# Kernel optimization log

Measured on AMD Instinct MI355X. Metric: run time of the kernel, lower is better.

## Reference

```python
import jax, jax.numpy as jnp
import numpy as np

N = 50000
E = 800000
IN = 128
H = 128
OUT = 64
L = 2
THETA = 1.0
SCALE = 2.0


def setup_inputs() -> dict:
    key = jax.random.key(0)
    ks = jax.random.split(key, 12)
    g = lambda k, s: (jax.random.normal(k, s, jnp.float32) * 0.05)
    return {
        "x": jax.random.normal(ks[0], (N, IN), jnp.float32),
        "edge_index": jax.random.randint(ks[1], (2, E), 0, N),
        "mlp_w1": g(ks[2], (IN, 512)), "mlp_b1": jnp.zeros((512,), jnp.float32),
        "mlp_w2": g(ks[3], (512, 64)), "mlp_b2": jnp.zeros((64,), jnp.float32),
        "mlp_w3": g(ks[4], (64, OUT)), "mlp_b3": jnp.zeros((OUT,), jnp.float32),
        "parsing": jnp.ones((L, OUT, OUT), jnp.float32) / SCALE,
        "lin0_w": g(ks[5], (IN, H)), "lin0_b": jnp.zeros((H,), jnp.float32),
        "lin1_w": g(ks[6], (H, OUT)), "lin1_b": jnp.zeros((OUT,), jnp.float32),
        "conv_w1": g(ks[7], (L, H, H)),
        "conv_w2": g(ks[8], (L, H, H)),
    }


def reference(x, edge_index, mlp_w1, mlp_b1, mlp_w2, mlp_b2, mlp_w3, mlp_b3,
              parsing, lin0_w, lin0_b, lin1_w, lin1_b, conv_w1, conv_w2):
    row, col = edge_index[0], edge_index[1]  # start, end

    # --- learn_soft_edge3 (algebraically exact reduction of outer-product + bmm + diag) ---
    h = jax.nn.relu(x @ mlp_w1 + mlp_b1)
    h = jax.nn.relu(h @ mlp_w2 + mlp_b2)
    logits = h @ mlp_w3 + mlp_b3                      # [N, OUT]
    P = jax.nn.relu(SCALE * parsing[0])               # [OUT, OUT]
    # diag(outer(start,end) @ P)[e,c] = start[e,c] * (end @ P)[e,c]
    ew = jnp.sum(logits[row] * (logits @ P)[col], axis=1)  # [E]
    mean = ew.mean()
    var = jnp.var(ew, ddof=1)                          # torch.var is unbiased
    ew = (ew - mean) * jnp.sqrt(jnp.float32(1e-4) / var) + 1.0

    # --- GCN2 stack ---
    x0 = jax.nn.relu(x @ lin0_w + lin0_b)              # [N, H]
    # gcn_norm with self loops (weight 1)
    loop = jnp.arange(N)
    r = jnp.concatenate([row, loop])
    c = jnp.concatenate([col, loop])
    w = jnp.concatenate([ew, jnp.ones((N,), ew.dtype)])
    deg = jax.ops.segment_sum(w, c, num_segments=N)
    dinv = jnp.where(deg > 0, jax.lax.rsqrt(jnp.where(deg > 0, deg, 1.0)), 0.0)
    norm = dinv[r] * w * dinv[c]                       # [E+N]

    hcur = x0
    alpha = 0.0
    for ln in range(L):
        agg = jax.ops.segment_sum(norm[:, None] * hcur[r], c, num_segments=N)  # [N, H]
        agg = agg * (1.0 - alpha)
        x0a = alpha * x0
        beta = float(np.log(THETA / (ln + 1) + 1.0))
        out = (1.0 - beta) * agg + beta * (agg @ conv_w1[ln]) \
            + (1.0 - beta) * x0a + beta * (x0a @ conv_w2[ln])
        hcur = jax.nn.relu(out)
    return hcur @ lin1_w + lin1_b                      # [N, OUT]
```

## Files before the change

### kernel.cpp

```cpp
#include <hip/hip_runtime.h>
#include <hip/hip_bf16.h>
#include <hip/hip_fp16.h>
#include <math.h>

#define NN 50000
#define NE 800000

typedef __attribute__((ext_vector_type(8))) short bf16x8;
typedef __attribute__((ext_vector_type(4))) float f32x4;

__device__ __forceinline__ short f2bf(float f){
  unsigned u = __float_as_uint(f);
  unsigned r = (u + 0x7fffu + ((u >> 16) & 1u)) >> 16;
  return (short)r;
}
__device__ __forceinline__ float bf2f(short s){
  return __uint_as_float(((unsigned)(unsigned short)s) << 16);
}

__device__ __forceinline__ unsigned f2fp8(float f){
  __half h = __float2half(f * 0.00390625f);
  unsigned hb = (unsigned)__half_as_ushort(h);
  unsigned s = hb >> 15;
  unsigned mag = hb & 0x7fffu;
  mag = mag + 0x3fu + ((mag >> 7) & 1u);
  unsigned m8 = mag >> 7;
  if (m8 > 0x7eu) m8 = 0x7eu;
  return (s << 7) | m8;
}
__device__ __forceinline__ void fp8x4_dec(unsigned u, float2& lo, float2& hi){
  unsigned l = ((u & 0x80u) << 8) | ((u & 0x7fu) << 7)
             | ((u & 0x8000u) << 16) | ((u & 0x7f00u) << 15);
  unsigned h = ((u & 0x800000u) >> 8) | ((u & 0x7f0000u) >> 9)
             | (u & 0x80000000u) | ((u & 0x7f000000u) >> 1);
  __half2 hl = *(__half2*)&l;
  __half2 hh = *(__half2*)&h;
  lo = __half22float2(hl);
  hi = __half22float2(hh);
}
__device__ __forceinline__ float fp8_dot4(unsigned a, unsigned b){
  float2 al, ah, bl, bh;
  fp8x4_dec(a, al, ah); fp8x4_dec(b, bl, bh);
  return al.x*bl.x + al.y*bl.y + ah.x*bh.x + ah.y*bh.y;
}

__global__ __launch_bounds__(256) void zero_cnt_k(int* __restrict__ cnt, float* __restrict__ scal, int n){
  int i = blockIdx.x*256 + threadIdx.x;
  if (i < n) cnt[i] = 0;
  if (blockIdx.x == 0 && threadIdx.x < 16) scal[threadIdx.x] = 0.0f;
}

__global__ __launch_bounds__(256) void prep_k(const float* __restrict__ w1,
    const float* __restrict__ w2, const float* __restrict__ w3, const float* __restrict__ pars,
    const float* __restrict__ lin0w, const float* __restrict__ cw1, const float* __restrict__ lin1w,
    short* __restrict__ w1t, short* __restrict__ w2t, short* __restrict__ w3t, short* __restrict__ Pt,
    short* __restrict__ lin0wt, short* __restrict__ cw1t0, short* __restrict__ cw1t1,
    short* __restrict__ lin1wt){
  int idx = blockIdx.x*256 + threadIdx.x;
  if (idx < 65536){
    int n = idx >> 7, k = idx & 127;
    w1t[idx] = f2bf(w1[k*512 + n]);
  } else if (idx < 98304){
    int i = idx - 65536; int n = i >> 9, k = i & 511;
    w2t[i] = f2bf(w2[k*64 + n]);
  } else if (idx < 102400){
    int i = idx - 98304; int n = i >> 6, k = i & 63;
    w3t[i] = f2bf(w3[k*64 + n]);
  } else if (idx < 106496){
    int i = idx - 102400; int n = i >> 6, k = i & 63;
    Pt[i] = f2bf(fmaxf(2.f*pars[k*64 + n], 0.f));
  } else if (idx < 122880){
    int i = idx - 106496; int n = i >> 7, k = i & 127;
    lin0wt[i] = f2bf(lin0w[k*128 + n]);
  } else if (idx < 139264){
    int i = idx - 122880; int n = i >> 7, k = i & 127;
    cw1t0[i] = f2bf(cw1[k*128 + n]);
  } else if (idx < 155648){
    int i = idx - 139264; int n = i >> 7, k = i & 127;
    cw1t1[i] = f2bf(cw1[16384 + k*128 + n]);
  } else if (idx < 163840){
    int i = idx - 155648; int n = i >> 7, k = i & 127;
    lin1wt[i] = f2bf(lin1w[k*64 + n]);
  }
}

__global__ __launch_bounds__(256) void mlp_mfma_k(
    const float* __restrict__ x,
    const short* __restrict__ w1t, const float* __restrict__ b1,
    const short* __restrict__ w2t, const float* __restrict__ b2,
    const short* __restrict__ w3t, const float* __restrict__ b3,
    const short* __restrict__ Pt,
    unsigned char* __restrict__ lg8, unsigned char* __restrict__ lgp8,
    short* __restrict__ xb, int M)
{
  __shared__ short xs [32][136];
  __shared__ short h1s[32][520];
  __shared__ short h2s[32][72];
  __shared__ short lgs[32][72];
  const int t = threadIdx.x;
  const int wave = t >> 6, lane = t & 63;
  const int quad = lane >> 4, l16 = lane & 15;
  const int m0 = blockIdx.x * 32;

  for (int task = t; task < 512; task += 256){
    int row = task >> 4, c0 = (task & 15) * 8;
    float4 v0 = make_float4(0,0,0,0), v1 = v0;
    if (m0 + row < M){
      v0 = *(const float4*)(x + (size_t)(m0+row)*128 + c0);
      v1 = *(const float4*)(x + (size_t)(m0+row)*128 + c0 + 4);
    }
    bf16x8 s;
    s[0]=f2bf(v0.x); s[1]=f2bf(v0.y); s[2]=f2bf(v0.z); s[3]=f2bf(v0.w);
    s[4]=f2bf(v1.x); s[5]=f2bf(v1.y); s[6]=f2bf(v1.z); s[7]=f2bf(v1.w);
    *(bf16x8*)&xs[row][c0] = s;
  }
  __syncthreads();

  {
    f32x4 acc[2][8];
    #pragma unroll
    for (int mt=0;mt<2;mt++)
      #pragma unroll
      for (int nt=0;nt<8;nt++) acc[mt][nt] = (f32x4){0.f,0.f,0.f,0.f};
    for (int k0 = 0; k0 < 128; k0 += 32){
      bf16x8 a0 = *(const bf16x8*)&xs[l16     ][k0 + quad*8];
      bf16x8 a1 = *(const bf16x8*)&xs[16 + l16][k0 + quad*8];
      #pragma unroll
      for (int nt = 0; nt < 8; nt++){
        int n = wave*128 + nt*16 + l16;
        bf16x8 b = *(const bf16x8*)(w1t + (size_t)n*128 + k0 + quad*8);
        acc[0][nt] = __builtin_amdgcn_mfma_f32_16x16x32_bf16(a0, b, acc[0][nt], 0,0,0);
        acc[1][nt] = __builtin_amdgcn_mfma_f32_16x16x32_bf16(a1, b, acc[1][nt], 0,0,0);
      }
    }
    #pragma unroll
    for (int nt = 0; nt < 8; nt++){
      int n = wave*128 + nt*16 + l16;
      float bb = b1[n];
      #pragma unroll
      for (int mt = 0; mt < 2; mt++){
        #pragma unroll
        for (int r = 0; r < 4; r++){
          int row = mt*16 + quad*4 + r;
          h1s[row][n] = f2bf(fmaxf(acc[mt][nt][r] + bb, 0.f));
        }
      }
    }
  }
  __syncthreads();

  {
    f32x4 acc[2];
    acc[0] = (f32x4){0.f,0.f,0.f,0.f}; acc[1] = acc[0];
    const int n = wave*16 + l16;
    for (int k0 = 0; k0 < 512; k0 += 32){
      bf16x8 b  = *(const bf16x8*)(w2t + (size_t)n*512 + k0 + quad*8);
      bf16x8 a0 = *(const bf16x8*)&h1s[l16     ][k0 + quad*8];
      bf16x8 a1 = *(const bf16x8*)&h1s[16 + l16][k0 + quad*8];
      acc[0] = __builtin_amdgcn_mfma_f32_16x16x32_bf16(a0, b, acc[0], 0,0,0);
      acc[1] = __builtin_amdgcn_mfma_f32_16x16x32_bf16(a1, b, acc[1], 0,0,0);
    }
    float bb = b2[n];
    #pragma unroll
    for (int mt = 0; mt < 2; mt++)
      #pragma unroll
      for (int r = 0; r < 4; r++)
        h2s[mt*16 + quad*4 + r][n] = f2bf(fmaxf(acc[mt][r] + bb, 0.f));
  }
  __syncthreads();

  {
    f32x4 acc[2];
    acc[0] = (f32x4){0.f,0.f,0.f,0.f}; acc[1] = acc[0];
    const int n = wave*16 + l16;
    for (int k0 = 0; k0 < 64; k0 += 32){
      bf16x8 b  = *(const bf16x8*)(w3t + (size_t)n*64 + k0 + quad*8);
      bf16x8 a0 = *(const bf16x8*)&h2s[l16     ][k0 + quad*8];
      bf16x8 a1 = *(const bf16x8*)&h2s[16 + l16][k0 + quad*8];
      acc[0] = __builtin_amdgcn_mfma_f32_16x16x32_bf16(a0, b, acc[0], 0,0,0);
      acc[1] = __builtin_amdgcn_mfma_f32_16x16x32_bf16(a1, b, acc[1], 0,0,0);
    }
    float bb = b3[n];
    #pragma unroll
    for (int mt = 0; mt < 2; mt++)
      #pragma unroll
      for (int r = 0; r < 4; r++)
        lgs[mt*16 + quad*4 + r][n] = f2bf(acc[mt][r] + bb);
  }
  __syncthreads();

  {
    f32x4 acc[2];
    acc[0] = (f32x4){0.f,0.f,0.f,0.f}; acc[1] = acc[0];
    const int n = wave*16 + l16;
    for (int k0 = 0; k0 < 64; k0 += 32){
      bf16x8 b  = *(const bf16x8*)(Pt + (size_t)n*64 + k0 + quad*8);
      bf16x8 a0 = *(const bf16x8*)&lgs[l16     ][k0 + quad*8];
      bf16x8 a1 = *(const bf16x8*)&lgs[16 + l16][k0 + quad*8];
      acc[0] = __builtin_amdgcn_mfma_f32_16x16x32_bf16(a0, b, acc[0], 0,0,0);
      acc[1] = __builtin_amdgcn_mfma_f32_16x16x32_bf16(a1, b, acc[1], 0,0,0);
    }
    #pragma unroll
    for (int mt = 0; mt < 2; mt++)
      #pragma unroll
      for (int r = 0; r < 4; r++)
        h2s[mt*16 + quad*4 + r][n] = f2bf(acc[mt][r]);
  }
  __syncthreads();

  {
    int row = t >> 3, c0 = (t & 7) * 8;
    int gm = m0 + row;
    if (gm < M){
      const short* pl = &lgs[row][c0];
      const short* pp = &h2s[row][c0];
      unsigned a0 = 0, a1 = 0, b0 = 0, b1 = 0;
      #pragma unroll
      for (int j = 0; j < 4; j++){
        a0 |= f2fp8(bf2f(pl[j]))     << (8*j);
        a1 |= f2fp8(bf2f(pl[4+j]))   << (8*j);
        b0 |= f2fp8(bf2f(pp[j]))     << (8*j);
        b1 |= f2fp8(bf2f(pp[4+j]))   << (8*j);
      }
      uint2 av; av.x = a0; av.y = a1;
      uint2 bv; bv.x = b0; bv.y = b1;
      *(uint2*)(lg8  + (size_t)gm*64 + c0) = av;
      *(uint2*)(lgp8 + (size_t)gm*64 + c0) = bv;
    }
  }
  for (int task = t; task < 512; task += 256){
    int row = task >> 4, c0 = (task & 15) * 8;
    int gm = m0 + row;
    if (gm < M)
      *(bf16x8*)(xb + (size_t)gm*128 + c0) = *(const bf16x8*)&xs[row][c0];
  }
}

template<int NT, bool RELU, bool RESID, bool BF16OUT>
__global__ __launch_bounds__(256) void bgemm_k(
    const short* __restrict__ A, const short* __restrict__ Bt,
    const float* __restrict__ bias, const short* __restrict__ extra,
    float* __restrict__ C, short* __restrict__ Cb, int M, float beta)
{
  const int N = NT*64;
  __shared__ short As[32][136];
  const int t = threadIdx.x;
  const int wave = t >> 6, lane = t & 63;
  const int quad = lane >> 4, l16 = lane & 15;
  const int m0 = blockIdx.x * 32;

  for (int task = t; task < 512; task += 256){
    int row = task >> 4, c0 = (task & 15) * 8;
    bf16x8 v = {0,0,0,0,0,0,0,0};
    if (m0 + row < M) v = *(const bf16x8*)(A + (size_t)(m0+row)*128 + c0);
    *(bf16x8*)&As[row][c0] = v;
  }
  __syncthreads();

  f32x4 acc[2][NT];
  #pragma unroll
  for (int mt=0;mt<2;mt++)
    #pragma unroll
    for (int nt=0;nt<NT;nt++) acc[mt][nt] = (f32x4){0.f,0.f,0.f,0.f};

  #pragma unroll
  for (int k0 = 0; k0 < 128; k0 += 32){
    bf16x8 a0 = *(const bf16x8*)&As[l16     ][k0 + quad*8];
    bf16x8 a1 = *(const bf16x8*)&As[16 + l16][k0 + quad*8];
    #pragma unroll
    for (int nt = 0; nt < NT; nt++){
      int n = (wave*NT + nt)*16 + l16;
      bf16x8 b = *(const bf16x8*)(Bt + (size_t)n*128 + k0 + quad*8);
      acc[0][nt] = __builtin_amdgcn_mfma_f32_16x16x32_bf16(a0, b, acc[0][nt], 0,0,0);
      acc[1][nt] = __builtin_amdgcn_mfma_f32_16x16x32_bf16(a1, b, acc[1][nt], 0,0,0);
    }
  }

  #pragma unroll
  for (int nt = 0; nt < NT; nt++){
    int n = (wave*NT + nt)*16 + l16;
    float bb = (bias != nullptr) ? bias[n] : 0.f;
    #pragma unroll
    for (int mt = 0; mt < 2; mt++){
      #pragma unroll
      for (int r = 0; r < 4; r++){
        int gm = m0 + mt*16 + quad*4 + r;
        if (gm >= M) continue;
        float v = acc[mt][nt][r];
        if (RESID){
          float ex = bf2f(extra[(size_t)gm*N + n]);
          v = beta*v + (1.f - beta)*ex;
        }
        v += bb;
        if (RELU) v = fmaxf(v, 0.f);
        if (BF16OUT) Cb[(size_t)gm*N + n] = f2bf(v);
        else         C [(size_t)gm*N + n] = v;
      }
    }
  }
}

__global__ __launch_bounds__(256) void count_k(const int* __restrict__ col, int* __restrict__ cnt, int E){
  int e = blockIdx.x*256 + threadIdx.x;
  if (e < E) atomicAdd(&cnt[col[e]], 1);
}

__global__ __launch_bounds__(256) void scan_sums_k(const int* __restrict__ cnt, int* __restrict__ bsum, int n){
  __shared__ int s[256];
  const int t = threadIdx.x;
  int i = blockIdx.x*1024 + t*4;
  int4 v = make_int4(0,0,0,0);
  if (i + 3 < n) v = *(const int4*)(cnt + i);
  else {
    if (i   < n) v.x = cnt[i];
    if (i+1 < n) v.y = cnt[i+1];
    if (i+2 < n) v.z = cnt[i+2];
    if (i+3 < n) v.w = cnt[i+3];
  }
  s[t] = v.x + v.y + v.z + v.w;
  __syncthreads();
  for (int st = 128; st; st >>= 1){
    if (t < st) s[t] += s[t + st];
    __syncthreads();
  }
  if (t == 0) bsum[blockIdx.x] = s[0];
}

__global__ __launch_bounds__(64) void scan_bsum_k(int* __restrict__ bsum, int nb){
  int t = threadIdx.x;
  int own = (t < nb) ? bsum[t] : 0;
  int v = own;
  #pragma unroll
  for (int off = 1; off < 64; off <<= 1){
    int o = __shfl_up(v, off, 64);
    if (t >= off) v += o;
  }
  if (t < nb) bsum[t] = v - own;
}

__global__ __launch_bounds__(256) void scan_final_k(const int* __restrict__ cnt, const int* __restrict__ bsum,
    int* __restrict__ off, int* __restrict__ cursor, int n, int total){
  __shared__ int s[256];
  const int t = threadIdx.x;
  int i = blockIdx.x*1024 + t*4;
  int4 v = make_int4(0,0,0,0);
  if (i + 3 < n) v = *(const int4*)(cnt + i);
  else {
    if (i   < n) v.x = cnt[i];
    if (i+1 < n) v.y = cnt[i+1];
    if (i+2 < n) v.z = cnt[i+2];
    if (i+3 < n) v.w = cnt[i+3];
  }
  int tsum = v.x + v.y + v.z + v.w;
  s[t] = tsum;
  __syncthreads();
  #pragma unroll
  for (int st = 1; st < 256; st <<= 1){
    int a = (t >= st) ? s[t - st] : 0;
    __syncthreads();
    s[t] += a;
    __syncthreads();
  }
  int base = s[t] - tsum + bsum[blockIdx.x];
  int o0 = base, o1 = o0 + v.x, o2 = o1 + v.y, o3 = o2 + v.z;
  if (i   < n){ off[i]   = o0; cursor[i]   = o0; }
  if (i+1 < n){ off[i+1] = o1; cursor[i+1] = o1; }
  if (i+2 < n){ off[i+2] = o2; cursor[i+2] = o2; }
  if (i+3 < n){ off[i+3] = o3; cursor[i+3] = o3; }
  if (blockIdx.x == 0 && t == 0) off[n] = total;
}

__global__ __launch_bounds__(256) void scatter_k(const int* __restrict__ row, const int* __restrict__ col,
    int* __restrict__ cursor, int* __restrict__ csr_src, int* __restrict__ csr_dst, int E){
  int e = blockIdx.x*256 + threadIdx.x;
  if (e < E){
    int r = row[e], c = col[e];
    int slot = atomicAdd(&cursor[c], 1);
    csr_src[slot] = r;
    csr_dst[slot] = c;
  }
}

__global__ __launch_bounds__(256) void ew2_k(const unsigned char* __restrict__ lg8,
    const unsigned char* __restrict__ lgp8,
    const int* __restrict__ src, const int* __restrict__ dst,
    float* __restrict__ w, float* __restrict__ scal, int E){
  const int t = threadIdx.x;
  const int lane = t & 63, wid = t >> 6;
  const int g = lane >> 4, q = lane & 15;
  const int gid = (blockIdx.x*4 + wid)*4 + g;
  const int ngroups = gridDim.x*16;
  float s = 0.f, ss = 0.f;
  for (int base = gid*4; base < E; base += ngroups*4){
    int4 r4 = *(const int4*)(src + base);
    int4 c4 = *(const int4*)(dst + base);
    unsigned a0 = *(const unsigned*)(lg8  + (size_t)r4.x*64 + q*4);
    unsigned a1 = *(const unsigned*)(lg8  + (size_t)r4.y*64 + q*4);
    unsigned a2 = *(const unsigned*)(lg8  + (size_t)r4.z*64 + q*4);
    unsigned a3 = *(const unsigned*)(lg8  + (size_t)r4.w*64 + q*4);
    unsigned b0 = *(const unsigned*)(lgp8 + (size_t)c4.x*64 + q*4);
    unsigned b1 = *(const unsigned*)(lgp8 + (size_t)c4.y*64 + q*4);
    unsigned b2 = *(const unsigned*)(lgp8 + (size_t)c4.z*64 + q*4);
    unsigned b3 = *(const unsigned*)(lgp8 + (size_t)c4.w*64 + q*4);
    float v0 = fp8_dot4(a0, b0);
    float v1 = fp8_dot4(a1, b1);
    float v2 = fp8_dot4(a2, b2);
    float v3 = fp8_dot4(a3, b3);
    #pragma unroll
    for (int o = 1; o < 16; o <<= 1){
      v0 += __shfl_xor(v0, o); v1 += __shfl_xor(v1, o);
      v2 += __shfl_xor(v2, o); v3 += __shfl_xor(v3, o);
    }
    if (q == 0){
      float4 vv = make_float4(v0*65536.f, v1*65536.f, v2*65536.f, v3*65536.f);
      *(float4*)(w + base) = vv;
      s  += vv.x + vv.y + vv.z + vv.w;
      ss += vv.x*vv.x + vv.y*vv.y + vv.z*vv.z + vv.w*vv.w;
    }
  }
  #pragma unroll
  for (int o = 1; o < 64; o <<= 1){ s += __shfl_xor(s, o); ss += __shfl_xor(ss, o); }
  __shared__ float ls[4], lss[4];
  if (lane == 0){ ls[wid] = s; lss[wid] = ss; }
  __syncthreads();
  if (t == 0){
    atomicAdd(&scal[0], ls[0]+ls[1]+ls[2]+ls[3]);
    atomicAdd(&scal[1], lss[0]+lss[1]+lss[2]+lss[3]);
  }
}

__global__ void finalize_k(float* scal, int E){
  double sum = (double)scal[0], sumsq = (double)scal[1];
  double mean = sum / (double)E;
  double var  = (sumsq - sum*sum/(double)E) / (double)(E-1);
  scal[2] = (float)mean;
  scal[3] = (float)sqrt(1e-4 / var);
}

__global__ __launch_bounds__(256) void degnorm_k(float* __restrict__ w, const int* __restrict__ off,
    const float* __restrict__ scal, float* __restrict__ dinv, int Nn){
  int n = blockIdx.x*256 + threadIdx.x;
  if (n < Nn){
    float mean = scal[2], k = scal[3];
    int s = off[n], e = off[n+1];
    float d = 1.0f;
    for (int j = s; j < e; j++){
      float v = (w[j] - mean) * k + 1.0f;
      w[j] = v;
      d += v;
    }
    dinv[n] = (d > 0.f) ? rsqrtf(d) : 0.f;
  }
}

__global__ __launch_bounds__(256) void wfin_k(float* __restrict__ w, const int* __restrict__ src,
    const int* __restrict__ dst, const float* __restrict__ dinv, int E){
  int e = blockIdx.x*256 + threadIdx.x;
  if (e < E) w[e] = w[e] * dinv[dst[e]] * dinv[src[e]];
}

__global__ __launch_bounds__(256) void agg_gather_k(const short* __restrict__ hb,
    const int* __restrict__ off, const int* __restrict__ src, const float* __restrict__ w,
    const float* __restrict__ dinv, short* __restrict__ aggb, int Nn){
  int n = blockIdx.x*4 + (threadIdx.x >> 6);
  int lane = threadIdx.x & 63;
  if (n >= Nn) return;
  float d = dinv[n];
  short2 hv = *(const short2*)(hb + (size_t)n*128 + lane*2);
  float acc0 = d*d*bf2f(hv.x), acc1 = d*d*bf2f(hv.y);
  int s = off[n], e = off[n+1];
  int j = s;
  for (; j + 7 < e; j += 8){
    int4 i0 = *(const int4*)(src + j);
    int4 i1 = *(const int4*)(src + j + 4);
    float4 w0 = *(const float4*)(w + j);
    float4 w1 = *(const float4*)(w + j + 4);
    short2 h0 = *(const short2*)(hb + (size_t)i0.x*128 + lane*2);
    short2 h1 = *(const short2*)(hb + (size_t)i0.y*128 + lane*2);
    short2 h2 = *(const short2*)(hb + (size_t)i0.z*128 + lane*2);
    short2 h3 = *(const short2*)(hb + (size_t)i0.w*128 + lane*2);
    short2 h4 = *(const short2*)(hb + (size_t)i1.x*128 + lane*2);
    short2 h5 = *(const short2*)(hb + (size_t)i1.y*128 + lane*2);
    short2 h6 = *(const short2*)(hb + (size_t)i1.z*128 + lane*2);
    short2 h7 = *(const short2*)(hb + (size_t)i1.w*128 + lane*2);
    acc0 += w0.x*bf2f(h0.x) + w0.y*bf2f(h1.x) + w0.z*bf2f(h2.x) + w0.w*bf2f(h3.x)
          + w1.x*bf2f(h4.x) + w1.y*bf2f(h5.x) + w1.z*bf2f(h6.x) + w1.w*bf2f(h7.x);
    acc1 += w0.x*bf2f(h0.y) + w0.y*bf2f(h1.y) + w0.z*bf2f(h2.y) + w0.w*bf2f(h3.y)
          + w1.x*bf2f(h4.y) + w1.y*bf2f(h5.y) + w1.z*bf2f(h6.y) + w1.w*bf2f(h7.y);
  }
  for (; j < e; j++){
    short2 h0 = *(const short2*)(hb + (size_t)src[j]*128 + lane*2);
    float w0 = w[j];
    acc0 += w0*bf2f(h0.x); acc1 += w0*bf2f(h0.y);
  }
  short2 o; o.x = f2bf(acc0); o.y = f2bf(acc1);
  *(short2*)(aggb + (size_t)n*128 + lane*2) = o;
}

extern "C" void kernel_launch(void* const* d_in, const int* in_sizes, int n_in,
                              void* d_out, int out_size, void* d_ws, size_t ws_size,
                              hipStream_t stream){
  const float* x      = (const float*)d_in[0];
  const int*   ei     = (const int*)  d_in[1];
  const float* w1     = (const float*)d_in[2];
  const float* b1     = (const float*)d_in[3];
  const float* w2     = (const float*)d_in[4];
  const float* b2     = (const float*)d_in[5];
  const float* w3     = (const float*)d_in[6];
  const float* b3     = (const float*)d_in[7];
  const float* pars   = (const float*)d_in[8];
  const float* lin0w  = (const float*)d_in[9];
  const float* lin0b  = (const float*)d_in[10];
  const float* lin1w  = (const float*)d_in[11];
  const float* lin1b  = (const float*)d_in[12];
  const float* cw1    = (const float*)d_in[13];
  float* out          = (float*)d_out;

  float* ws = (float*)d_ws;
  int*   cnt     = (int*)(ws + 0);
  int*   off     = (int*)(ws + 50048);
  int*   cursor  = (int*)(ws + 100096);
  int*   csr_src = (int*)(ws + 150144);
  float* csr_w   = ws + 950144;
  int*   bsum    = (int*)(ws + 1750400);
  short* lin0wt  = (short*)(ws + 1751000);
  short* cw1t0   = lin0wt + 16384;
  short* cw1t1   = cw1t0 + 16384;
  short* lin1wt  = cw1t1 + 16384;
  unsigned char* lg8  = (unsigned char*)(ws + 1800000);
  unsigned char* lgp8 = (unsigned char*)(ws + 2600000);
  float* dinv    = ws + 5800000;
  float* scal    = ws + 5850048;
  short* bufAb   = (short*)(ws + 5900000);
  short* bufCb   = (short*)(ws + 9100000);
  short* aggb    = (short*)(ws + 12300000);
  short* bufBb   = (short*)(ws + 15500000);
  short* w1t     = (short*)(ws + 18700000);
  short* w2t     = w1t + 65536;
  short* w3t     = w2t + 32768;
  short* Pt      = w3t + 4096;
  short* xb      = (short*)(ws + 18800000);
  int*   csr_dst = (int*)(ws + 22000000);

  const int Mn = NN, E = NE;
  const int* erow = ei;
  const int* ecol = ei + E;
  const float beta0 = 0.69314718055994530942f;
  const float beta1 = 0.40546510810816438198f;
  const int nScanB = (Mn + 1023) / 1024;
  const int nGB = (Mn + 31) / 32;

  zero_cnt_k<<<(Mn+255)/256, 256, 0, stream>>>(cnt, scal, Mn);
  prep_k<<<(163840+255)/256, 256, 0, stream>>>(w1, w2, w3, pars, lin0w, cw1, lin1w,
                                               w1t, w2t, w3t, Pt, lin0wt, cw1t0, cw1t1, lin1wt);
  count_k<<<(E+255)/256, 256, 0, stream>>>(ecol, cnt, E);
  scan_sums_k<<<nScanB, 256, 0, stream>>>(cnt, bsum, Mn);
  scan_bsum_k<<<1, 64, 0, stream>>>(bsum, nScanB);
  scan_final_k<<<nScanB, 256, 0, stream>>>(cnt, bsum, off, cursor, Mn, E);
  scatter_k<<<(E+255)/256, 256, 0, stream>>>(erow, ecol, cursor, csr_src, csr_dst, E);
  mlp_mfma_k<<<(Mn+31)/32, 256, 0, stream>>>(x, w1t, b1, w2t, b2, w3t, b3, Pt,
                                             lg8, lgp8, xb, Mn);
  ew2_k<<<1024, 256, 0, stream>>>(lg8, lgp8, csr_src, csr_dst, csr_w, scal, E);
  finalize_k<<<1, 1, 0, stream>>>(scal, E);
  degnorm_k<<<(Mn+255)/256, 256, 0, stream>>>(csr_w, off, scal, dinv, Mn);
  wfin_k<<<(E+255)/256, 256, 0, stream>>>(csr_w, csr_src, csr_dst, dinv, E);
  bgemm_k<2,true,false,true><<<nGB, 256, 0, stream>>>(xb, lin0wt, lin0b, nullptr, nullptr, bufAb, Mn, 0.f);
  agg_gather_k<<<(Mn+3)/4, 256, 0, stream>>>(bufAb, off, csr_src, csr_w, dinv, aggb, Mn);
  bgemm_k<2,true,true,true><<<nGB, 256, 0, stream>>>(aggb, cw1t0, nullptr, aggb, nullptr, bufCb, Mn, beta0);
  agg_gather_k<<<(Mn+3)/4, 256, 0, stream>>>(bufCb, off, csr_src, csr_w, dinv, aggb, Mn);
  bgemm_k<2,true,true,true><<<nGB, 256, 0, stream>>>(aggb, cw1t1, nullptr, aggb, nullptr, bufBb, Mn, beta1);
  bgemm_k<1,false,false,false><<<nGB, 256, 0, stream>>>(bufBb, lin1wt, lin1b, nullptr, out, nullptr, Mn, 0.f);
}
```

Before: 430.9 us.

## Split fused MLP into parallel first-layer GEMM and tail kernel

The fused MLP kernel is split in two. One kernel computes the 512-wide first hidden layer over a 2D grid that tiles the output columns, and writes it to global memory as bf16. A second kernel reads it back for the remaining layers and the fp8 logit packing. This is meant to raise parallelism and occupancy by dropping the large shared-memory hidden buffer, at the cost of an extra round trip of the hidden activations through global memory.

```diff
diff --git a/kernel.cpp b/kernel.cpp
--- a/kernel.cpp
+++ b/kernel.cpp
@@ -84,17 +84,82 @@
   }
 }
 
-__global__ __launch_bounds__(256) void mlp_mfma_k(
-    const float* __restrict__ x,
-    const short* __restrict__ w1t, const float* __restrict__ b1,
+__global__ __launch_bounds__(256) void h1_gemm_k(
+    const float* __restrict__ x, const short* __restrict__ w1t, const float* __restrict__ b1,
+    short* __restrict__ h1b, short* __restrict__ xb, int M)
+{
+  __shared__ short xs[32][136];
+  const int t = threadIdx.x;
+  const int wave = t >> 6, lane = t & 63;
+  const int quad = lane >> 4, l16 = lane & 15;
+  const int m0 = blockIdx.x * 32;
+  const int n0 = blockIdx.y * 128;
+
+  for (int task = t; task < 512; task += 256){
+    int row = task >> 4, c0 = (task & 15) * 8;
+    float4 v0 = make_float4(0,0,0,0), v1 = v0;
+    if (m0 + row < M){
+      v0 = *(const float4*)(x + (size_t)(m0+row)*128 + c0);
+      v1 = *(const float4*)(x + (size_t)(m0+row)*128 + c0 + 4);
+    }
+    bf16x8 s;
+    s[0]=f2bf(v0.x); s[1]=f2bf(v0.y); s[2]=f2bf(v0.z); s[3]=f2bf(v0.w);
+    s[4]=f2bf(v1.x); s[5]=f2bf(v1.y); s[6]=f2bf(v1.z); s[7]=f2bf(v1.w);
+    *(bf16x8*)&xs[row][c0] = s;
+  }
+  __syncthreads();
+
+  if (blockIdx.y == 0){
+    for (int task = t; task < 512; task += 256){
+      int row = task >> 4, c0 = (task & 15) * 8;
+      int gm = m0 + row;
+      if (gm < M)
+        *(bf16x8*)(xb + (size_t)gm*128 + c0) = *(const bf16x8*)&xs[row][c0];
+    }
+  }
+
+  f32x4 acc[2][2];
+  #pragma unroll
+  for (int mt=0;mt<2;mt++)
+    #pragma unroll
+    for (int nt=0;nt<2;nt++) acc[mt][nt] = (f32x4){0.f,0.f,0.f,0.f};
+
+  #pragma unroll
+  for (int k0 = 0; k0 < 128; k0 += 32){
+    bf16x8 a0 = *(const bf16x8*)&xs[l16     ][k0 + quad*8];
+    bf16x8 a1 = *(const bf16x8*)&xs[16 + l16][k0 + quad*8];
+    #pragma unroll
+    for (int nt = 0; nt < 2; nt++){
+      int n = n0 + (wave*2 + nt)*16 + l16;
+      bf16x8 b = *(const bf16x8*)(w1t + (size_t)n*128 + k0 + quad*8);
+      acc[0][nt] = __builtin_amdgcn_mfma_f32_16x16x32_bf16(a0, b, acc[0][nt], 0,0,0);
+      acc[1][nt] = __builtin_amdgcn_mfma_f32_16x16x32_bf16(a1, b, acc[1][nt], 0,0,0);
+    }
+  }
+
+  #pragma unroll
+  for (int nt = 0; nt < 2; nt++){
+    int n = n0 + (wave*2 + nt)*16 + l16;
+    float bb = b1[n];
+    #pragma unroll
+    for (int mt = 0; mt < 2; mt++){
+      #pragma unroll
+      for (int r = 0; r < 4; r++){
+        int gm = m0 + mt*16 + quad*4 + r;
+        if (gm >= M) continue;
+        h1b[(size_t)gm*512 + n] = f2bf(fmaxf(acc[mt][nt][r] + bb, 0.f));
+      }
+    }
+  }
+}
+
+__global__ __launch_bounds__(256) void mlp_tail_k(
+    const short* __restrict__ h1b,
     const short* __restrict__ w2t, const float* __restrict__ b2,
     const short* __restrict__ w3t, const float* __restrict__ b3,
     const short* __restrict__ Pt,
-    unsigned char* __restrict__ lg8, unsigned char* __restrict__ lgp8,
-    short* __restrict__ xb, int M)
+    unsigned char* __restrict__ lg8, unsigned char* __restrict__ lgp8, int M)
 {
-  __shared__ short xs [32][136];
-  __shared__ short h1s[32][520];
   __shared__ short h2s[32][72];
   __shared__ short lgs[32][72];
   const int t = threadIdx.x;
@@ -102,61 +167,16 @@
   const int quad = lane >> 4, l16 = lane & 15;
   const int m0 = blockIdx.x * 32;
 
-  for (int task = t; task < 512; task += 256){
-    int row = task >> 4, c0 = (task & 15) * 8;
-    float4 v0 = make_float4(0,0,0,0), v1 = v0;
-    if (m0 + row < M){
-      v0 = *(const float4*)(x + (size_t)(m0+row)*128 + c0);
-      v1 = *(const float4*)(x + (size_t)(m0+row)*128 + c0 + 4);
-    }
-    bf16x8 s;
-    s[0]=f2bf(v0.x); s[1]=f2bf(v0.y); s[2]=f2bf(v0.z); s[3]=f2bf(v0.w);
-    s[4]=f2bf(v1.x); s[5]=f2bf(v1.y); s[6]=f2bf(v1.z); s[7]=f2bf(v1.w);
-    *(bf16x8*)&xs[row][c0] = s;
-  }
-  __syncthreads();
-
-  {
-    f32x4 acc[2][8];
-    #pragma unroll
-    for (int mt=0;mt<2;mt++)
-      #pragma unroll
-      for (int nt=0;nt<8;nt++) acc[mt][nt] = (f32x4){0.f,0.f,0.f,0.f};
-    for (int k0 = 0; k0 < 128; k0 += 32){
-      bf16x8 a0 = *(const bf16x8*)&xs[l16     ][k0 + quad*8];
-      bf16x8 a1 = *(const bf16x8*)&xs[16 + l16][k0 + quad*8];
-      #pragma unroll
-      for (int nt = 0; nt < 8; nt++){
-        int n = wave*128 + nt*16 + l16;
-        bf16x8 b = *(const bf16x8*)(w1t + (size_t)n*128 + k0 + quad*8);
-        acc[0][nt] = __builtin_amdgcn_mfma_f32_16x16x32_bf16(a0, b, acc[0][nt], 0,0,0);
-        acc[1][nt] = __builtin_amdgcn_mfma_f32_16x16x32_bf16(a1, b, acc[1][nt], 0,0,0);
-      }
-    }
-    #pragma unroll
-    for (int nt = 0; nt < 8; nt++){
-      int n = wave*128 + nt*16 + l16;
-      float bb = b1[n];
-      #pragma unroll
-      for (int mt = 0; mt < 2; mt++){
-        #pragma unroll
-        for (int r = 0; r < 4; r++){
-          int row = mt*16 + quad*4 + r;
-          h1s[row][n] = f2bf(fmaxf(acc[mt][nt][r] + bb, 0.f));
-        }
-      }
-    }
-  }
-  __syncthreads();
-
   {
     f32x4 acc[2];
     acc[0] = (f32x4){0.f,0.f,0.f,0.f}; acc[1] = acc[0];
     const int n = wave*16 + l16;
+    const size_t row0 = (size_t)(m0 + l16) * 512;
+    const size_t row1 = (size_t)(m0 + 16 + l16) * 512;
     for (int k0 = 0; k0 < 512; k0 += 32){
       bf16x8 b  = *(const bf16x8*)(w2t + (size_t)n*512 + k0 + quad*8);
-      bf16x8 a0 = *(const bf16x8*)&h1s[l16     ][k0 + quad*8];
-      bf16x8 a1 = *(const bf16x8*)&h1s[16 + l16][k0 + quad*8];
+      bf16x8 a0 = *(const bf16x8*)(h1b + row0 + k0 + quad*8);
+      bf16x8 a1 = *(const bf16x8*)(h1b + row1 + k0 + quad*8);
       acc[0] = __builtin_amdgcn_mfma_f32_16x16x32_bf16(a0, b, acc[0], 0,0,0);
       acc[1] = __builtin_amdgcn_mfma_f32_16x16x32_bf16(a1, b, acc[1], 0,0,0);
     }
@@ -227,12 +247,6 @@
       *(uint2*)(lg8  + (size_t)gm*64 + c0) = av;
       *(uint2*)(lgp8 + (size_t)gm*64 + c0) = bv;
     }
-  }
-  for (int task = t; task < 512; task += 256){
-    int row = task >> 4, c0 = (task & 15) * 8;
-    int gm = m0 + row;
-    if (gm < M)
-      *(bf16x8*)(xb + (size_t)gm*128 + c0) = *(const bf16x8*)&xs[row][c0];
   }
 }
 
@@ -535,6 +549,7 @@
   short* bufCb   = (short*)(ws + 9100000);
   short* aggb    = (short*)(ws + 12300000);
   short* bufBb   = (short*)(ws + 15500000);
+  short* h1b     = (short*)(ws + 5900000);
   short* w1t     = (short*)(ws + 18700000);
   short* w2t     = w1t + 65536;
   short* w3t     = w2t + 32768;
@@ -558,8 +573,8 @@
   scan_bsum_k<<<1, 64, 0, stream>>>(bsum, nScanB);
   scan_final_k<<<nScanB, 256, 0, stream>>>(cnt, bsum, off, cursor, Mn, E);
   scatter_k<<<(E+255)/256, 256, 0, stream>>>(erow, ecol, cursor, csr_src, csr_dst, E);
-  mlp_mfma_k<<<(Mn+31)/32, 256, 0, stream>>>(x, w1t, b1, w2t, b2, w3t, b3, Pt,
-                                             lg8, lgp8, xb, Mn);
+  h1_gemm_k<<<dim3(nGB, 4), 256, 0, stream>>>(x, w1t, b1, h1b, xb, Mn);
+  mlp_tail_k<<<nGB, 256, 0, stream>>>(h1b, w2t, b2, w3t, b3, Pt, lg8, lgp8, Mn);
   ew2_k<<<1024, 256, 0, stream>>>(lg8, lgp8, csr_src, csr_dst, csr_w, scal, E);
   finalize_k<<<1, 1, 0, stream>>>(scal, E);
   degnorm_k<<<(Mn+255)/256, 256, 0, stream>>>(csr_w, off, scal, dinv, Mn);
```

Measured after the change: 470.5 us. +9.2%, slower.
